# Kernel optimization log

Hardware: AMD Instinct MI355X
Metric: run time of the kernel (lower is better)

## Reference

```python
import jax, jax.numpy as jnp
import numpy as np

B, S, C, H = 2, 2048, 512, 16
D = C // H  # 32
SQRT_DIM = float(np.sqrt(C))  # module scales by sqrt(in_channels), not sqrt(dim)


def setup_inputs() -> dict:
    key = jax.random.key(0)
    ks = jax.random.split(key, 16)
    sc = 1.0 / np.sqrt(C)
    f32 = jnp.float32
    return {
        "q": jax.random.normal(ks[0], (B, S, C), f32),
        "k": jax.random.normal(ks[1], (B, S, C), f32),
        "v": jax.random.normal(ks[2], (B, S, C), f32),
        "pos_embedding": jax.random.normal(ks[3], (B, S, C), f32),
        "Wq": jax.random.normal(ks[4], (C, C), f32) * sc,
        "bq": jnp.zeros((C,), f32),
        "Wk": jax.random.normal(ks[5], (C, C), f32) * sc,
        "bk": jnp.zeros((C,), f32),
        "Wv": jax.random.normal(ks[6], (C, C), f32) * sc,
        "bv": jnp.zeros((C,), f32),
        "Wp": jax.random.normal(ks[7], (C, C), f32) * sc,  # pos_proj has no bias
        "u_bias": jax.random.normal(ks[8], (H, D), f32) * 0.1,
        "v_bias": jax.random.normal(ks[9], (H, D), f32) * 0.1,
        "Wo": jax.random.normal(ks[10], (C, C), f32) * sc,
        "bo": jnp.zeros((C,), f32),
    }


def _skew(pos_score):
    # Transformer-XL pad-shift trick: [B,H,S1,S2] -> relative-shifted scores
    b, h, s1, s2 = pos_score.shape
    zeros = jnp.zeros((b, h, s1, 1), pos_score.dtype)
    padded = jnp.concatenate([zeros, pos_score], axis=-1)  # [b,h,s1,s2+1]
    padded = padded.reshape(b, h, s2 + 1, s1)
    return padded[:, :, 1:].reshape(b, h, s1, s2)


def reference(q, k, v, pos_embedding, Wq, bq, Wk, bk, Wv, bv, Wp, u_bias, v_bias, Wo, bo):
    query = (q @ Wq.T + bq).reshape(B, S, H, D)      # [B,S,H,D]
    key_ = (k @ Wk.T + bk).reshape(B, S, H, D)
    value = (v @ Wv.T + bv).reshape(B, S, H, D)
    pos = (pos_embedding @ Wp.T).reshape(B, S, H, D)
    content = jnp.einsum('bshd,bthd->bhst', query + u_bias, key_)   # [B,H,S,S]
    pos_score = _skew(jnp.einsum('bshd,bthd->bhst', query + v_bias, pos))
    score = (content + pos_score) / SQRT_DIM
    attn = jax.nn.softmax(score, axis=-1)            # dropout_p=0 (eval)
    context = jnp.einsum('bhst,bthd->bshd', attn, value).reshape(B, S, C)
    return context @ Wo.T + bo
```

## Files before the change

### kernel.cpp

```cpp
#include <hip/hip_runtime.h>
#include <math.h>

#define S_ 2048
#define C_ 512
#define H_ 16
#define D_ 32
#define B_ 2
#define M_ (B_ * S_)
#define RSCALE 0.04419417382415922f

typedef __attribute__((ext_vector_type(8))) short bf16x8;
typedef __attribute__((ext_vector_type(4))) float f32x4;

__device__ inline unsigned short f2bf(float f) {
  unsigned u = __builtin_bit_cast(unsigned, f);
  u += 0x7FFFu + ((u >> 16) & 1u);
  return (unsigned short)(u >> 16);
}

__global__ __launch_bounds__(256) void split_x4(
    const float* __restrict__ q, const float* __restrict__ k,
    const float* __restrict__ v, const float* __restrict__ pe,
    short* __restrict__ xb) {
  const int z = blockIdx.y;
  const float* src = z == 0 ? q : z == 1 ? k : z == 2 ? v : pe;
  const size_t off = (size_t)z * M_ * C_;
  const size_t i = ((size_t)blockIdx.x * 256 + threadIdx.x) * 4;
  float4 f = *(const float4*)(src + i);
  float ff[4] = {f.x, f.y, f.z, f.w};
  ushort4 hv;
  unsigned short* ph = (unsigned short*)&hv;
#pragma unroll
  for (int e = 0; e < 4; ++e) ph[e] = f2bf(ff[e]);
  *(ushort4*)(xb + off + i) = hv;
}

__global__ __launch_bounds__(256) void split_w(
    const float* __restrict__ w0, const float* __restrict__ w1,
    const float* __restrict__ w2, const float* __restrict__ w3,
    const float* __restrict__ w4, short* __restrict__ wb,
    short* __restrict__ woh, short* __restrict__ wol) {
  const int z = blockIdx.y;
  const float* src = z == 0 ? w0 : z == 1 ? w1 : z == 2 ? w2 : z == 3 ? w3 : w4;
  const size_t i = ((size_t)blockIdx.x * 256 + threadIdx.x) * 4;
  float4 f = *(const float4*)(src + i);
  float ff[4] = {f.x, f.y, f.z, f.w};
  if (z < 4) {
    const size_t off = (size_t)z * C_ * C_;
    ushort4 hv;
    unsigned short* ph = (unsigned short*)&hv;
#pragma unroll
    for (int e = 0; e < 4; ++e) ph[e] = f2bf(ff[e]);
    *(ushort4*)(wb + off + i) = hv;
  } else {
    ushort4 hv, lv;
    unsigned short* ph = (unsigned short*)&hv;
    unsigned short* pl = (unsigned short*)&lv;
#pragma unroll
    for (int e = 0; e < 4; ++e) {
      unsigned u = __builtin_bit_cast(unsigned, ff[e]);
      unsigned hi = u & 0xffff0000u;
      ph[e] = (unsigned short)(hi >> 16);
      pl[e] = f2bf(ff[e] - __builtin_bit_cast(float, hi));
    }
    *(ushort4*)(woh + i) = hv;
    *(ushort4*)(wol + i) = lv;
  }
}

__global__ __launch_bounds__(256) void proj4(
    const short* __restrict__ XB, const short* __restrict__ W4,
    const float* __restrict__ bq, const float* __restrict__ bkk,
    const float* __restrict__ bvv, const float* __restrict__ ub,
    const float* __restrict__ vb, short* __restrict__ QU,
    short* __restrict__ QV, short* __restrict__ Kb, short* __restrict__ Vt,
    short* __restrict__ POS) {
  const int z = blockIdx.z;
  const short* X = XB + (size_t)z * M_ * C_;
  const short* W = W4 + (size_t)z * C_ * C_;
  const int tid = threadIdx.x;
  const int w = tid >> 6, lane = tid & 63, col = lane & 15, quad = lane >> 4;
  const int bm = blockIdx.y * 128, bn = blockIdx.x * 64;
  const f32x4 zc = {0.f, 0.f, 0.f, 0.f};
  f32x4 acc[2][4] = {{zc, zc, zc, zc}, {zc, zc, zc, zc}};
  const short* Xr0 = X + (size_t)(bm + 32 * w + col) * C_ + quad * 8;
  const short* Xr1 = Xr0 + 16 * C_;
  const short* Wr = W + (size_t)(bn + col) * C_ + quad * 8;
#pragma unroll 4
  for (int kt = 0; kt < 16; ++kt) {
    const int k = kt * 32;
    const bf16x8 a0 = *(const bf16x8*)(Xr0 + k);
    const bf16x8 a1 = *(const bf16x8*)(Xr1 + k);
#pragma unroll
    for (int j = 0; j < 4; ++j) {
      const bf16x8 b = *(const bf16x8*)(Wr + (size_t)(16 * j) * C_ + k);
      acc[0][j] = __builtin_amdgcn_mfma_f32_16x16x32_bf16(a0, b, acc[0][j], 0, 0, 0);
      acc[1][j] = __builtin_amdgcn_mfma_f32_16x16x32_bf16(a1, b, acc[1][j], 0, 0, 0);
    }
  }
  const float* b1 = z == 0 ? bq : z == 1 ? bkk : z == 2 ? bvv : nullptr;
#pragma unroll
  for (int mt = 0; mt < 2; ++mt) {
#pragma unroll
    for (int j = 0; j < 4; ++j) {
      const int gn = bn + 16 * j + col;
      const int h = gn >> 5, d0 = gn & 31;
#pragma unroll
      for (int r = 0; r < 4; ++r) {
        const int gm = bm + 32 * w + 16 * mt + quad * 4 + r;
        const int bb = gm >> 11, s = gm & (S_ - 1);
        const float a = acc[mt][j][r] + (b1 ? b1[gn] : 0.0f);
        if (z == 0) {
          const size_t base = ((size_t)(bb * H_ + h) * S_ + s) * D_ + d0;
          QU[base] = (short)f2bf(a + ub[gn]);
          QV[base] = (short)f2bf(a + vb[gn]);
        } else if (z == 1) {
          Kb[((size_t)(bb * H_ + h) * S_ + s) * D_ + d0] = (short)f2bf(a);
        } else if (z == 2) {
          Vt[((size_t)(bb * H_ + h) * D_ + d0) * S_ + s] = (short)f2bf(a);
        } else {
          POS[((size_t)(bb * H_ + h) * S_ + s) * D_ + d0] = (short)f2bf(a);
        }
      }
    }
  }
}

__global__ __launch_bounds__(256) void gemm_out(
    const short* __restrict__ CTXh, const short* __restrict__ CTXl,
    const short* __restrict__ WOh, const short* __restrict__ WOl,
    const float* __restrict__ bo, float* __restrict__ out) {
  const int tid = threadIdx.x;
  const int w = tid >> 6, lane = tid & 63, col = lane & 15, quad = lane >> 4;
  const int bm = blockIdx.y * 128, bn = blockIdx.x * 64;
  const f32x4 zc = {0.f, 0.f, 0.f, 0.f};
  f32x4 acc[2][4] = {{zc, zc, zc, zc}, {zc, zc, zc, zc}};
  const size_t a0off = (size_t)(bm + 32 * w + col) * C_ + quad * 8;
  const size_t a1off = a0off + (size_t)16 * C_;
  const size_t boff = (size_t)(bn + col) * C_ + quad * 8;
#pragma unroll 2
  for (int kt = 0; kt < 16; ++kt) {
    const int k = kt * 32;
    const bf16x8 ah0 = *(const bf16x8*)(CTXh + a0off + k);
    const bf16x8 al0 = *(const bf16x8*)(CTXl + a0off + k);
    const bf16x8 ah1 = *(const bf16x8*)(CTXh + a1off + k);
    const bf16x8 al1 = *(const bf16x8*)(CTXl + a1off + k);
#pragma unroll
    for (int j = 0; j < 4; ++j) {
      const size_t bo_ = boff + (size_t)(16 * j) * C_ + k;
      const bf16x8 bh = *(const bf16x8*)(WOh + bo_);
      const bf16x8 bl = *(const bf16x8*)(WOl + bo_);
      acc[0][j] = __builtin_amdgcn_mfma_f32_16x16x32_bf16(ah0, bh, acc[0][j], 0, 0, 0);
      acc[0][j] = __builtin_amdgcn_mfma_f32_16x16x32_bf16(ah0, bl, acc[0][j], 0, 0, 0);
      acc[0][j] = __builtin_amdgcn_mfma_f32_16x16x32_bf16(al0, bh, acc[0][j], 0, 0, 0);
      acc[1][j] = __builtin_amdgcn_mfma_f32_16x16x32_bf16(ah1, bh, acc[1][j], 0, 0, 0);
      acc[1][j] = __builtin_amdgcn_mfma_f32_16x16x32_bf16(ah1, bl, acc[1][j], 0, 0, 0);
      acc[1][j] = __builtin_amdgcn_mfma_f32_16x16x32_bf16(al1, bh, acc[1][j], 0, 0, 0);
    }
  }
#pragma unroll
  for (int mt = 0; mt < 2; ++mt) {
#pragma unroll
    for (int j = 0; j < 4; ++j) {
      const int gn = bn + 16 * j + col;
#pragma unroll
      for (int r = 0; r < 4; ++r) {
        const int gm = bm + 32 * w + 16 * mt + quad * 4 + r;
        out[(size_t)gm * C_ + gn] = acc[mt][j][r] + bo[gn];
      }
    }
  }
}

__global__ __launch_bounds__(256, 4) void attn_mfma(
    const short* __restrict__ QU, const short* __restrict__ QV,
    const short* __restrict__ Kb, const short* __restrict__ Vt,
    const short* __restrict__ POSb, short* __restrict__ CTXh,
    short* __restrict__ CTXl) {
  __shared__ float PB[64 * 128];
  __shared__ short Pl[64 * 64];
  const int tid = threadIdx.x;
  const int w = tid >> 6;
  const int lane = tid & 63;
  const int col = lane & 15;
  const int quad = lane >> 4;
  const int m0 = blockIdx.x * 64;
  const int bh = blockIdx.y;
  const int b = bh >> 4, h = bh & 15;

  const short* QUh = QU + (size_t)bh * S_ * D_;
  const short* QVh = QV + (size_t)bh * S_ * D_;
  const short* Kh = Kb + (size_t)bh * S_ * D_;
  const short* Vh = Vt + (size_t)bh * D_ * S_;
  const short* Ph = POSb + (size_t)bh * S_ * D_;

  const int arow = m0 + 16 * w + col;
  const bf16x8 aQU = *(const bf16x8*)(QUh + (size_t)arow * D_ + quad * 8);
  const bf16x8 aQVA = *(const bf16x8*)(QVh + (size_t)arow * D_ + quad * 8);
  const bf16x8 aQVB = *(const bf16x8*)(QVh + (size_t)(arow + 1) * D_ + quad * 8);

  const f32x4 zc = {0.f, 0.f, 0.f, 0.f};
  const bf16x8 zb = {0, 0, 0, 0, 0, 0, 0, 0};
  f32x4 ctxa0 = zc, ctxa1 = zc;
  float lpart[4] = {0.f, 0.f, 0.f, 0.f};
  const int mi0 = 16 * w + 4 * quad;

  for (int ch = 0; ch < 32; ++ch) {
    const int n0 = ch * 64;
    const int dnm = n0 - m0;
    f32x4 sc[4];
#pragma unroll
    for (int j = 0; j < 4; ++j) {
      bf16x8 bk = *(const bf16x8*)(Kh + (size_t)(n0 + 16 * j + col) * D_ + quad * 8);
      sc[j] = __builtin_amdgcn_mfma_f32_16x16x32_bf16(aQU, bk, zc, 0, 0, 0);
    }
    if (dnm <= 63) {
      const int tA0 = S_ - 64 + dnm;
#pragma unroll
      for (int j = 0; j < 8; ++j) {
        const int t = tA0 + 16 * j + col;
        bf16x8 bp = *(const bf16x8*)(Ph + (long)t * D_ + quad * 8);
        if (t >= S_) bp = zb;
        f32x4 c = __builtin_amdgcn_mfma_f32_16x16x32_bf16(aQVA, bp, zc, 0, 0, 0);
#pragma unroll
        for (int r = 0; r < 4; ++r) {
          const int mi = mi0 + r;
          const int cc = (16 * j + col) ^ (((mi & 4) << 2) ^ ((mi & 3) << 3));
          PB[mi * 128 + cc] = c[r];
        }
      }
      __syncthreads();
#pragma unroll
      for (int j = 0; j < 4; ++j)
#pragma unroll
        for (int r = 0; r < 4; ++r) {
          const int mi = mi0 + r;
          const int nj = 16 * j + col;
          if (dnm + nj - mi <= 0) {
            const int idx = (nj - mi + 63) ^ (((mi & 4) << 2) ^ ((mi & 3) << 3));
            sc[j][r] += PB[mi * 128 + idx];
          }
        }
    }
    if (dnm >= -61) {
      __syncthreads();
      const int tB0 = dnm - 65;
#pragma unroll
      for (int j = 0; j < 8; ++j) {
        const int t = tB0 + 16 * j + col;
        bf16x8 bp = *(const bf16x8*)(Ph + (long)t * D_ + quad * 8);
        if (t < 0) bp = zb;
        f32x4 c = __builtin_amdgcn_mfma_f32_16x16x32_bf16(aQVB, bp, zc, 0, 0, 0);
#pragma unroll
        for (int r = 0; r < 4; ++r) {
          const int mi = mi0 + r;
          const int cc = (16 * j + col) ^ (((mi & 4) << 2) ^ ((mi & 3) << 3));
          PB[mi * 128 + cc] = c[r];
        }
      }
      __syncthreads();
#pragma unroll
      for (int j = 0; j < 4; ++j)
#pragma unroll
        for (int r = 0; r < 4; ++r) {
          const int mi = mi0 + r;
          const int nj = 16 * j + col;
          if (dnm + nj - mi >= 2) {
            const int idx = (nj - mi + 63) ^ (((mi & 4) << 2) ^ ((mi & 3) << 3));
            sc[j][r] += PB[mi * 128 + idx];
          }
        }
    }
    __syncthreads();
#pragma unroll
    for (int j = 0; j < 4; ++j)
#pragma unroll
      for (int r = 0; r < 4; ++r) {
        const float p = __expf(sc[j][r] * RSCALE);
        lpart[r] += p;
        const int mi = mi0 + r;
        const int cc = (16 * j + col) ^ ((mi & 7) << 3);
        Pl[mi * 64 + cc] = (short)f2bf(p);
      }
    __syncthreads();
    const int prow = 16 * w + col;
    const int psw = (prow & 7) << 3;
#pragma unroll
    for (int k0 = 0; k0 < 2; ++k0) {
      const bf16x8 ap = *(const bf16x8*)(&Pl[prow * 64 + ((k0 * 32 + quad * 8) ^ psw)]);
      bf16x8 bv0 = *(const bf16x8*)(Vh + (size_t)col * S_ + n0 + k0 * 32 + quad * 8);
      ctxa0 = __builtin_amdgcn_mfma_f32_16x16x32_bf16(ap, bv0, ctxa0, 0, 0, 0);
      bf16x8 bv1 = *(const bf16x8*)(Vh + (size_t)(16 + col) * S_ + n0 + k0 * 32 + quad * 8);
      ctxa1 = __builtin_amdgcn_mfma_f32_16x16x32_bf16(ap, bv1, ctxa1, 0, 0, 0);
    }
  }
#pragma unroll
  for (int r = 0; r < 4; ++r) {
    float s = lpart[r];
    s += __shfl_xor(s, 1);
    s += __shfl_xor(s, 2);
    s += __shfl_xor(s, 4);
    s += __shfl_xor(s, 8);
    lpart[r] = 1.0f / s;
  }
  const int mrow = m0 + mi0;
#pragma unroll
  for (int r = 0; r < 4; ++r) {
    const size_t obase = ((size_t)(b * S_ + mrow + r)) * C_ + h * D_;
    const float v0 = ctxa0[r] * lpart[r];
    const float v1 = ctxa1[r] * lpart[r];
    const unsigned u0 = __builtin_bit_cast(unsigned, v0) & 0xffff0000u;
    const unsigned u1 = __builtin_bit_cast(unsigned, v1) & 0xffff0000u;
    CTXh[obase + col] = (short)(u0 >> 16);
    CTXl[obase + col] = (short)f2bf(v0 - __builtin_bit_cast(float, u0));
    CTXh[obase + 16 + col] = (short)(u1 >> 16);
    CTXl[obase + 16 + col] = (short)f2bf(v1 - __builtin_bit_cast(float, u1));
  }
}

extern "C" void kernel_launch(void* const* d_in, const int* in_sizes, int n_in,
                              void* d_out, int out_size, void* d_ws, size_t ws_size,
                              hipStream_t stream) {
  (void)in_sizes; (void)n_in; (void)out_size; (void)ws_size;
  const float* q = (const float*)d_in[0];
  const float* k = (const float*)d_in[1];
  const float* v = (const float*)d_in[2];
  const float* pe = (const float*)d_in[3];
  const float* Wq = (const float*)d_in[4];
  const float* bq = (const float*)d_in[5];
  const float* Wk = (const float*)d_in[6];
  const float* bk = (const float*)d_in[7];
  const float* Wv = (const float*)d_in[8];
  const float* bv = (const float*)d_in[9];
  const float* Wp = (const float*)d_in[10];
  const float* ub = (const float*)d_in[11];
  const float* vb = (const float*)d_in[12];
  const float* Wo = (const float*)d_in[13];
  const float* bo = (const float*)d_in[14];
  float* out = (float*)d_out;

  const size_t MC = (size_t)M_ * C_;
  const size_t WC = (size_t)C_ * C_;
  short* XB = (short*)d_ws;
  short* W4 = XB + 4 * MC;
  short* WOh = W4 + 4 * WC;
  short* WOl = WOh + WC;
  short* QUb = WOl + WC;
  short* QVb = QUb + MC;
  short* Kbb = QVb + MC;
  short* Vtb = Kbb + MC;
  short* POSB = Vtb + MC;
  short* CTXh = POSB + MC;
  short* CTXl = CTXh + MC;

  split_x4<<<dim3(2048, 4), 256, 0, stream>>>(q, k, v, pe, XB);
  split_w<<<dim3(256, 5), 256, 0, stream>>>(Wq, Wk, Wv, Wp, Wo, W4, WOh, WOl);
  proj4<<<dim3(8, 32, 4), 256, 0, stream>>>(XB, W4, bq, bk, bv, ub, vb,
                                            QUb, QVb, Kbb, Vtb, POSB);
  attn_mfma<<<dim3(S_ / 64, B_ * H_), 256, 0, stream>>>(QUb, QVb, Kbb, Vtb, POSB,
                                                        CTXh, CTXl);
  gemm_out<<<dim3(8, 32), 256, 0, stream>>>(CTXh, CTXl, WOh, WOl, bo, out);
}
```

Measured before the change: 381.3 us.

## Merge conversion kernels, halve GEMM blocks, cut band-score barriers in attention

Merges the two fp32-to-bf16 conversion kernels into one launch. Shrinks the projection and output GEMM blocks to 128 threads with 64-row tiles, doubling the grid. In attention, both positional halves now write disjoint masked regions of the shared band buffer, and the band term is read once during the exponent step. This drops several __syncthreads and the zero-masking selects. The wasted y-grid blocks in the merged conversion launch exit early but still cost launch slots, and the disjoint-write masking must exactly match the old conditions.

Measured after the change: 425.3 us. 11.5% more time.

```diff
diff --git a/kernel.cpp b/kernel.cpp
--- a/kernel.cpp
+++ b/kernel.cpp
@@ -18,41 +18,41 @@
   return (unsigned short)(u >> 16);
 }
 
-__global__ __launch_bounds__(256) void split_x4(
+__global__ __launch_bounds__(256) void convert(
     const float* __restrict__ q, const float* __restrict__ k,
     const float* __restrict__ v, const float* __restrict__ pe,
-    short* __restrict__ xb) {
-  const int z = blockIdx.y;
-  const float* src = z == 0 ? q : z == 1 ? k : z == 2 ? v : pe;
-  const size_t off = (size_t)z * M_ * C_;
-  const size_t i = ((size_t)blockIdx.x * 256 + threadIdx.x) * 4;
-  float4 f = *(const float4*)(src + i);
-  float ff[4] = {f.x, f.y, f.z, f.w};
-  ushort4 hv;
-  unsigned short* ph = (unsigned short*)&hv;
-#pragma unroll
-  for (int e = 0; e < 4; ++e) ph[e] = f2bf(ff[e]);
-  *(ushort4*)(xb + off + i) = hv;
-}
-
-__global__ __launch_bounds__(256) void split_w(
-    const float* __restrict__ w0, const float* __restrict__ w1,
-    const float* __restrict__ w2, const float* __restrict__ w3,
-    const float* __restrict__ w4, short* __restrict__ wb,
-    short* __restrict__ woh, short* __restrict__ wol) {
-  const int z = blockIdx.y;
-  const float* src = z == 0 ? w0 : z == 1 ? w1 : z == 2 ? w2 : z == 3 ? w3 : w4;
-  const size_t i = ((size_t)blockIdx.x * 256 + threadIdx.x) * 4;
-  float4 f = *(const float4*)(src + i);
-  float ff[4] = {f.x, f.y, f.z, f.w};
-  if (z < 4) {
-    const size_t off = (size_t)z * C_ * C_;
+    const float* __restrict__ Wq, const float* __restrict__ Wk,
+    const float* __restrict__ Wv, const float* __restrict__ Wp,
+    const float* __restrict__ Wo, short* __restrict__ XB,
+    short* __restrict__ W4, short* __restrict__ WOh, short* __restrict__ WOl) {
+  const int y = blockIdx.y;
+  if (y < 4) {
+    const float* src = y == 0 ? q : y == 1 ? k : y == 2 ? v : pe;
+    const size_t i = ((size_t)blockIdx.x * 256 + threadIdx.x) * 4;
+    float4 f = *(const float4*)(src + i);
+    float ff[4] = {f.x, f.y, f.z, f.w};
     ushort4 hv;
     unsigned short* ph = (unsigned short*)&hv;
 #pragma unroll
     for (int e = 0; e < 4; ++e) ph[e] = f2bf(ff[e]);
-    *(ushort4*)(wb + off + i) = hv;
+    *(ushort4*)(XB + (size_t)y * M_ * C_ + i) = hv;
+  } else if (y == 4) {
+    if (blockIdx.x >= 1024) return;
+    const int z = blockIdx.x >> 8, blk = blockIdx.x & 255;
+    const float* src = z == 0 ? Wq : z == 1 ? Wk : z == 2 ? Wv : Wp;
+    const size_t i = ((size_t)blk * 256 + threadIdx.x) * 4;
+    float4 f = *(const float4*)(src + i);
+    float ff[4] = {f.x, f.y, f.z, f.w};
+    ushort4 hv;
+    unsigned short* ph = (unsigned short*)&hv;
+#pragma unroll
+    for (int e = 0; e < 4; ++e) ph[e] = f2bf(ff[e]);
+    *(ushort4*)(W4 + (size_t)z * C_ * C_ + i) = hv;
   } else {
+    if (blockIdx.x >= 256) return;
+    const size_t i = ((size_t)blockIdx.x * 256 + threadIdx.x) * 4;
+    float4 f = *(const float4*)(Wo + i);
+    float ff[4] = {f.x, f.y, f.z, f.w};
     ushort4 hv, lv;
     unsigned short* ph = (unsigned short*)&hv;
     unsigned short* pl = (unsigned short*)&lv;
@@ -63,12 +63,12 @@
       ph[e] = (unsigned short)(hi >> 16);
       pl[e] = f2bf(ff[e] - __builtin_bit_cast(float, hi));
     }
-    *(ushort4*)(woh + i) = hv;
-    *(ushort4*)(wol + i) = lv;
-  }
-}
-
-__global__ __launch_bounds__(256) void proj4(
+    *(ushort4*)(WOh + i) = hv;
+    *(ushort4*)(WOl + i) = lv;
+  }
+}
+
+__global__ __launch_bounds__(128) void proj4(
     const short* __restrict__ XB, const short* __restrict__ W4,
     const float* __restrict__ bq, const float* __restrict__ bkk,
     const float* __restrict__ bvv, const float* __restrict__ ub,
@@ -80,7 +80,7 @@
   const short* W = W4 + (size_t)z * C_ * C_;
   const int tid = threadIdx.x;
   const int w = tid >> 6, lane = tid & 63, col = lane & 15, quad = lane >> 4;
-  const int bm = blockIdx.y * 128, bn = blockIdx.x * 64;
+  const int bm = blockIdx.y * 64, bn = blockIdx.x * 64;
   const f32x4 zc = {0.f, 0.f, 0.f, 0.f};
   f32x4 acc[2][4] = {{zc, zc, zc, zc}, {zc, zc, zc, zc}};
   const short* Xr0 = X + (size_t)(bm + 32 * w + col) * C_ + quad * 8;
@@ -126,13 +126,13 @@
   }
 }
 
-__global__ __launch_bounds__(256) void gemm_out(
+__global__ __launch_bounds__(128) void gemm_out(
     const short* __restrict__ CTXh, const short* __restrict__ CTXl,
     const short* __restrict__ WOh, const short* __restrict__ WOl,
     const float* __restrict__ bo, float* __restrict__ out) {
   const int tid = threadIdx.x;
   const int w = tid >> 6, lane = tid & 63, col = lane & 15, quad = lane >> 4;
-  const int bm = blockIdx.y * 128, bn = blockIdx.x * 64;
+  const int bm = blockIdx.y * 64, bn = blockIdx.x * 64;
   const f32x4 zc = {0.f, 0.f, 0.f, 0.f};
   f32x4 acc[2][4] = {{zc, zc, zc, zc}, {zc, zc, zc, zc}};
   const size_t a0off = (size_t)(bm + 32 * w + col) * C_ + quad * 8;
@@ -200,10 +200,10 @@
   const bf16x8 aQVB = *(const bf16x8*)(QVh + (size_t)(arow + 1) * D_ + quad * 8);
 
   const f32x4 zc = {0.f, 0.f, 0.f, 0.f};
-  const bf16x8 zb = {0, 0, 0, 0, 0, 0, 0, 0};
   f32x4 ctxa0 = zc, ctxa1 = zc;
   float lpart[4] = {0.f, 0.f, 0.f, 0.f};
   const int mi0 = 16 * w + 4 * quad;
+  const int swz0 = ((mi0 & 4) << 2) ^ ((mi0 & 3) << 3);
 
   for (int ch = 0; ch < 32; ++ch) {
     const int n0 = ch * 64;
@@ -220,67 +220,44 @@
       for (int j = 0; j < 8; ++j) {
         const int t = tA0 + 16 * j + col;
         bf16x8 bp = *(const bf16x8*)(Ph + (long)t * D_ + quad * 8);
-        if (t >= S_) bp = zb;
         f32x4 c = __builtin_amdgcn_mfma_f32_16x16x32_bf16(aQVA, bp, zc, 0, 0, 0);
-#pragma unroll
-        for (int r = 0; r < 4; ++r) {
-          const int mi = mi0 + r;
-          const int cc = (16 * j + col) ^ (((mi & 4) << 2) ^ ((mi & 3) << 3));
-          PB[mi * 128 + cc] = c[r];
+        const int cc = 16 * j + col;
+        if (cc <= 63 - dnm) {
+#pragma unroll
+          for (int r = 0; r < 4; ++r)
+            PB[(mi0 + r) * 128 + (cc ^ (swz0 ^ (r << 3)))] = c[r];
         }
       }
-      __syncthreads();
-#pragma unroll
-      for (int j = 0; j < 4; ++j)
-#pragma unroll
-        for (int r = 0; r < 4; ++r) {
-          const int mi = mi0 + r;
-          const int nj = 16 * j + col;
-          if (dnm + nj - mi <= 0) {
-            const int idx = (nj - mi + 63) ^ (((mi & 4) << 2) ^ ((mi & 3) << 3));
-            sc[j][r] += PB[mi * 128 + idx];
-          }
-        }
     }
     if (dnm >= -61) {
-      __syncthreads();
       const int tB0 = dnm - 65;
 #pragma unroll
       for (int j = 0; j < 8; ++j) {
         const int t = tB0 + 16 * j + col;
         bf16x8 bp = *(const bf16x8*)(Ph + (long)t * D_ + quad * 8);
-        if (t < 0) bp = zb;
         f32x4 c = __builtin_amdgcn_mfma_f32_16x16x32_bf16(aQVB, bp, zc, 0, 0, 0);
-#pragma unroll
-        for (int r = 0; r < 4; ++r) {
-          const int mi = mi0 + r;
-          const int cc = (16 * j + col) ^ (((mi & 4) << 2) ^ ((mi & 3) << 3));
-          PB[mi * 128 + cc] = c[r];
+        const int cc = 16 * j + col;
+        if (cc >= 65 - dnm) {
+#pragma unroll
+          for (int r = 0; r < 4; ++r)
+            PB[(mi0 + r) * 128 + (cc ^ (swz0 ^ (r << 3)))] = c[r];
         }
       }
-      __syncthreads();
-#pragma unroll
-      for (int j = 0; j < 4; ++j)
-#pragma unroll
-        for (int r = 0; r < 4; ++r) {
-          const int mi = mi0 + r;
-          const int nj = 16 * j + col;
-          if (dnm + nj - mi >= 2) {
-            const int idx = (nj - mi + 63) ^ (((mi & 4) << 2) ^ ((mi & 3) << 3));
-            sc[j][r] += PB[mi * 128 + idx];
-          }
-        }
     }
     __syncthreads();
 #pragma unroll
     for (int j = 0; j < 4; ++j)
 #pragma unroll
       for (int r = 0; r < 4; ++r) {
-        const float p = __expf(sc[j][r] * RSCALE);
+        const int mi = mi0 + r;
+        const int nj = 16 * j + col;
+        const int u = dnm + nj - mi;
+        float bandv = 0.0f;
+        if (u <= 0 || u >= 2)
+          bandv = PB[mi * 128 + ((nj - mi + 63) ^ (swz0 ^ (r << 3)))];
+        const float p = __expf((sc[j][r] + bandv) * RSCALE);
         lpart[r] += p;
-        const int mi = mi0 + r;
-        const int cc = (16 * j + col) ^ ((mi & 7) << 3);
-        Pl[mi * 64 + cc] = (short)f2bf(p);
+        Pl[mi * 64 + ((16 * j + col) ^ ((mi & 7) << 3))] = (short)f2bf(p);
       }
     __syncthreads();
     const int prow = 16 * w + col;
@@ -353,11 +330,11 @@
   short* CTXh = POSB + MC;
   short* CTXl = CTXh + MC;
 
-  split_x4<<<dim3(2048, 4), 256, 0, stream>>>(q, k, v, pe, XB);
-  split_w<<<dim3(256, 5), 256, 0, stream>>>(Wq, Wk, Wv, Wp, Wo, W4, WOh, WOl);
-  proj4<<<dim3(8, 32, 4), 256, 0, stream>>>(XB, W4, bq, bk, bv, ub, vb,
+  convert<<<dim3(2048, 6), 256, 0, stream>>>(q, k, v, pe, Wq, Wk, Wv, Wp, Wo,
+                                             XB, W4, WOh, WOl);
+  proj4<<<dim3(8, 64, 4), 128, 0, stream>>>(XB, W4, bq, bk, bv, ub, vb,
                                             QUb, QVb, Kbb, Vtb, POSB);
   attn_mfma<<<dim3(S_ / 64, B_ * H_), 256, 0, stream>>>(QUb, QVb, Kbb, Vtb, POSB,
                                                         CTXh, CTXl);
-  gemm_out<<<dim3(8, 32), 256, 0, stream>>>(CTXh, CTXl, WOh, WOl, bo, out);
-}
+  gemm_out<<<dim3(8, 64), 128, 0, stream>>>(CTXh, CTXl, WOh, WOl, bo, out);
+}
```
